# Kernel optimization log

Hardware: AMD Instinct MI355X
Metric: run time of the kernel (lower is better)

The kernel has to match this reference:

```python
import jax, jax.numpy as jnp
import numpy as np

N, A, C = 4, 8732, 81
SCALE_XY, SCALE_WH = 0.1, 0.2   # dboxes.scale_xy / scale_wh; Loss uses reciprocals
LAM, W_IOU = 1.0, 0.01
EPS_IOU = float(np.finfo(float).eps)


def setup_inputs() -> dict:
    key = jax.random.key(0)
    ks = jax.random.split(key, 8)
    ploc = jax.random.normal(ks[0], (N, 4, A), dtype=jnp.float32) * 0.5
    plabel = jax.random.normal(ks[1], (N, C, A), dtype=jnp.float32)
    # ground-truth loc in xywh with strictly positive wh (loc_vec takes a log)
    gxy = jax.random.uniform(ks[2], (N, 2, A), dtype=jnp.float32)
    gwh = jax.random.uniform(ks[3], (N, 2, A), dtype=jnp.float32) * 0.4 + 0.05
    gloc = jnp.concatenate([gxy, gwh], axis=1)
    lab = jax.random.randint(ks[4], (N, A), 1, C)
    keep = jax.random.uniform(ks[5], (N, A)) < 0.02
    glabel = jnp.where(keep, lab, 0).astype(jnp.int32)
    # default boxes in xywh, shape [1, 4, A]
    dxy = jax.random.uniform(ks[6], (1, 2, A), dtype=jnp.float32)
    dwh = jax.random.uniform(ks[7], (1, 2, A), dtype=jnp.float32) * 0.45 + 0.05
    dboxes = jnp.concatenate([dxy, dwh], axis=1)
    return {"ploc": ploc, "plabel": plabel, "gloc": gloc, "glabel": glabel, "dboxes": dboxes}


def _decode_ltrb(loc, dboxes):
    """scale_back_batch: encoded [N,4,A] + dboxes xywh [1,4,A] -> ltrb [N,A,4]."""
    b = jnp.transpose(loc, (0, 2, 1))      # [N, A, 4]
    d = jnp.transpose(dboxes, (0, 2, 1))   # [1, A, 4]
    xy = SCALE_XY * b[..., :2] * d[..., 2:] + d[..., :2]
    wh = jnp.exp(SCALE_WH * b[..., 2:]) * d[..., 2:]
    return jnp.concatenate([xy - 0.5 * wh, xy + 0.5 * wh], axis=-1)


def _iou_sum(p, g):
    """p, g: [A,4] ltrb -> per-anchor sum over all g boxes of IoU(p_i, g_k)."""
    area_p = (p[:, 2] - p[:, 0]) * (p[:, 3] - p[:, 1])
    area_g = (g[:, 2] - g[:, 0]) * (g[:, 3] - g[:, 1])
    iw = jnp.maximum(jnp.minimum(p[:, None, 2], g[None, :, 2]) - jnp.maximum(p[:, None, 0], g[None, :, 0]), 0.0)
    ih = jnp.maximum(jnp.minimum(p[:, None, 3], g[None, :, 3]) - jnp.maximum(p[:, None, 1], g[None, :, 1]), 0.0)
    inter = iw * ih                                      # [A, A]
    ua = jnp.maximum(area_p[:, None] + area_g[None, :] - inter, EPS_IOU)
    return (inter / ua).sum(axis=1)                      # [A]


def _forward(ploc, plabel, gloc, glabel, dboxes):
    mask = glabel > 0                                    # [N, A]
    pos_num = mask.sum(axis=1)                           # [N]

    # loc_vec: encode ground truth against default boxes
    dxy, dwh = dboxes[:, :2, :], dboxes[:, 2:, :]
    gxy_t = (1.0 / SCALE_XY) * (gloc[:, :2, :] - dxy) / dwh
    gwh_t = (1.0 / SCALE_WH) * jnp.log(gloc[:, 2:, :] / dwh)
    vec_gd = jnp.concatenate([gxy_t, gwh_t], axis=1)     # [N, 4, A]

    # SmoothL1 (beta=1), summed over coord dim
    diff = ploc - vec_gd
    ad = jnp.abs(diff)
    sl1 = jnp.where(ad < 1.0, 0.5 * diff * diff, ad - 0.5).sum(axis=1)  # [N, A]

    # per-anchor cross entropy
    logp = jax.nn.log_softmax(plabel, axis=1)            # [N, C, A]
    con = -jnp.take_along_axis(logp, glabel[:, None, :], axis=1)[:, 0, :]  # [N, A]

    # weighted-IoU reweighting (weights are detached in the original)
    p_ltrb = _decode_ltrb(ploc, dboxes)                  # [N, A, 4]
    g_ltrb = _decode_ltrb(gloc, dboxes)
    iou_s = jax.vmap(_iou_sum)(p_ltrb, g_ltrb)           # [N, A]
    valid = (p_ltrb[..., 0] < p_ltrb[..., 2]) & (p_ltrb[..., 1] < p_ltrb[..., 3])
    weights = jnp.where(valid, W_IOU * iou_s ** LAM, 0.0)
    weights = jax.lax.stop_gradient(weights)
    sl1 = (sl1 / (sl1 + weights)) * sl1

    sl1_pos = (mask.astype(sl1.dtype) * sl1).sum(axis=1)  # [N]

    # hard negative mining: double argsort for ranks
    con_neg = jnp.where(mask, 0.0, con)
    con_idx = jnp.argsort(-con_neg, axis=1)
    con_rank = jnp.argsort(con_idx, axis=1)
    neg_num = jnp.minimum(3 * pos_num, A)[:, None]
    neg_mask = con_rank < neg_num
    closs = (con * (mask.astype(con.dtype) + neg_mask.astype(con.dtype))).sum(axis=1)

    total = sl1_pos + closs
    num_mask = (pos_num > 0).astype(total.dtype)
    pn = jnp.maximum(pos_num.astype(total.dtype), 1e-6)
    return (total * num_mask / pn).mean()


def reference(ploc, plabel, gloc, glabel, dboxes):
    return _forward(ploc, plabel, gloc, glabel, dboxes)
```

## Files before the change

### kernel.cpp

```cpp
#include <hip/hip_runtime.h>
#include <math.h>

#define A_N 8732
#define NAT (4 * A_N)
#define BATCH 4
#define CLS 81
#define TILE 256
#define PTHREADS 512
#define SEG 128
#define ABLKP 69
#define NBINS 2048
#define PLB 128

__device__ __forceinline__ float sl1f(float d) {
    float ad = fabsf(d);
    return ad < 1.0f ? 0.5f * d * d : ad - 0.5f;
}
__device__ __forceinline__ unsigned umap(float v) {
    return __float_as_uint(v) | 0x80000000u;
}

__device__ void suffix_find(const int* lcnt, const float* lsum, int k, int tid,
                            int* ic, float* fsum,
                            int* o_b, int* o_krem, float* o_sumA)
{
    int base = tid * 8;
    int cs = 0; float ss = 0.0f;
    #pragma unroll
    for (int j = 0; j < 8; j++) { cs += lcnt[base + j]; ss += lsum[base + j]; }
    ic[tid] = cs; fsum[tid] = ss;
    __syncthreads();
    for (int off = 1; off < TILE; off <<= 1) {
        int v = ic[tid]; float f = fsum[tid];
        int v2 = 0; float f2 = 0.0f;
        if (tid + off < TILE) { v2 = ic[tid + off]; f2 = fsum[tid + off]; }
        __syncthreads();
        ic[tid] = v + v2; fsum[tid] = f + f2;
        __syncthreads();
    }
    int run = ic[tid] - cs;
    float runs = fsum[tid] - ss;
    for (int j = 7; j >= 0; j--) {
        int b = base + j; int c = lcnt[b];
        if (run < k && run + c >= k) { *o_b = b; *o_krem = k - run; *o_sumA = runs; }
        run += c; runs += lsum[b];
    }
    __syncthreads();
}

__global__ __launch_bounds__(PTHREADS) void prep_kernel(
    const float* __restrict__ ploc, const float* __restrict__ plabel,
    const float* __restrict__ gloc, const int* __restrict__ glabel,
    const float* __restrict__ dboxes,
    float4* __restrict__ pbox, float4* __restrict__ gbox,
    float* __restrict__ sl1raw, float* __restrict__ conneg,
    int* __restrict__ poslist,
    int* __restrict__ poscnt,
    float* __restrict__ consum,
    float* __restrict__ out)
{
    __shared__ float sh_se[4][SEG];
    __shared__ float sh_xg[4][SEG];
    __shared__ int   wcnt[2];
    __shared__ float wsum[2];
    const int t   = threadIdx.x;
    const int blk = blockIdx.x;
    const int n   = blockIdx.y;
    const int i     = t & (SEG - 1);
    const int chunk = t >> 7;
    const int a = blk * SEG + i;

    if (t == 0 && blk == 0 && n == 0) *out = 0.0f;

    int lab = 0;
    float se = 0.0f, xv = 0.0f;
    if (a < A_N) {
        lab = glabel[n * A_N + a];
        const float* pb = plabel + (size_t)n * CLS * A_N + a;
        const int c0 = chunk * 20 + (chunk > 0 ? 1 : 0);
        const int c1 = c0 + (chunk == 0 ? 21 : 20);
        #pragma unroll 21
        for (int c = c0; c < c1; c++) {
            float x = pb[(size_t)c * A_N];
            se += expf(x);
            xv = (c == lab) ? x : xv;
        }
    }
    sh_se[chunk][i] = se;
    sh_xg[chunk][i] = xv;
    __syncthreads();

    bool msk = false;
    float cv = 0.0f;
    if (t < SEG && a < A_N) {
        float set = sh_se[0][i] + sh_se[1][i] + sh_se[2][i] + sh_se[3][i];
        float xg  = sh_xg[0][i] + sh_xg[1][i] + sh_xg[2][i] + sh_xg[3][i];
        cv = logf(set) - xg;
        msk = lab > 0;
        conneg[n * A_N + a] = msk ? 0.0f : cv;

        float d0 = dboxes[0*A_N+a], d1 = dboxes[1*A_N+a], d2 = dboxes[2*A_N+a], d3 = dboxes[3*A_N+a];
        const float* pl = ploc + (size_t)n * 4 * A_N;
        const float* gl = gloc + (size_t)n * 4 * A_N;
        float p0 = pl[0*A_N+a], p1 = pl[1*A_N+a], p2 = pl[2*A_N+a], p3 = pl[3*A_N+a];
        float g0 = gl[0*A_N+a], g1 = gl[1*A_N+a], g2 = gl[2*A_N+a], g3 = gl[3*A_N+a];

        float v0 = 10.0f * (g0 - d0) / d2;
        float v1 = 10.0f * (g1 - d1) / d3;
        float v2 = 5.0f * logf(g2 / d2);
        float v3 = 5.0f * logf(g3 / d3);
        sl1raw[n * A_N + a] = sl1f(p0-v0) + sl1f(p1-v1) + sl1f(p2-v2) + sl1f(p3-v3);

        float cx = 0.1f*p0*d2 + d0, cy = 0.1f*p1*d3 + d1;
        float cw = expf(0.2f*p2)*d2, ch = expf(0.2f*p3)*d3;
        pbox[(size_t)n*A_N + a] = make_float4(cx-0.5f*cw, cy-0.5f*ch, cx+0.5f*cw, cy+0.5f*ch);
        float ex = 0.1f*g0*d2 + d0, ey = 0.1f*g1*d3 + d1;
        float ew = expf(0.2f*g2)*d2, eh = expf(0.2f*g3)*d3;
        gbox[(size_t)n*A_N + a] = make_float4(ex-0.5f*ew, ey-0.5f*eh, ex+0.5f*ew, ey+0.5f*eh);
    }

    unsigned long long bal = __ballot(msk);
    int wid = t >> 6, lane = t & 63;
    float wv = msk ? cv : 0.0f;
    #pragma unroll
    for (int off = 32; off > 0; off >>= 1) wv += __shfl_down(wv, off);
    if (t < SEG && lane == 0) { wcnt[wid] = __popcll(bal); wsum[wid] = wv; }
    __syncthreads();
    if (msk) {
        int base = (wid == 1) ? wcnt[0] : 0;
        int off = base + (int)__popcll(bal & ((1ULL << lane) - 1ULL));
        poslist[(n * ABLKP + blk) * SEG + off] = a;
    }
    if (t == 0) {
        poscnt[n * ABLKP + blk] = wcnt[0] + wcnt[1];
        consum[n * ABLKP + blk] = wsum[0] + wsum[1];
    }
}

__global__ __launch_bounds__(TILE) void tail_kernel(
    const float4* __restrict__ pbox, const float4* __restrict__ gbox,
    const float* __restrict__ sl1raw, const float* __restrict__ conneg,
    const int* __restrict__ poslist, const int* __restrict__ poscnt,
    const float* __restrict__ consum,
    float* __restrict__ out)
{
    __shared__ int   spre[ABLKP + 1];
    __shared__ float r4[4];
    const int n = blockIdx.y, tid = threadIdx.x;

    if (tid == 0) {
        int run = 0;
        #pragma unroll
        for (int s = 0; s < ABLKP; s++) { spre[s] = run; run += poscnt[n * ABLKP + s]; }
        spre[ABLKP] = run;
    }
    __syncthreads();
    const int np = spre[ABLKP];
    if (np <= 0) return;
    const float inv = 1.0f / ((float)np * (float)BATCH);

    if (blockIdx.x < PLB) {
        for (int p = blockIdx.x; p < np; p += PLB) {
            int s = 0;
            while (spre[s + 1] <= p) s++;
            int a = poslist[(n * ABLKP + s) * SEG + (p - spre[s])];
            float4 b = pbox[(size_t)n * A_N + a];
            float ap = (b.z - b.x) * (b.w - b.y);
            float acc = 0.0f;
            for (int k = tid; k < A_N; k += TILE) {
                float4 g = gbox[(size_t)n * A_N + k];
                float iw = fmaxf(fminf(b.z, g.z) - fmaxf(b.x, g.x), 0.0f);
                float ih = fmaxf(fminf(b.w, g.w) - fmaxf(b.y, g.y), 0.0f);
                float inter = iw * ih;
                float ua = ap + (g.z - g.x) * (g.w - g.y) - inter;
                acc += inter * __builtin_amdgcn_rcpf(ua);
            }
            #pragma unroll
            for (int off = 32; off > 0; off >>= 1) acc += __shfl_down(acc, off);
            if ((tid & 63) == 0) r4[tid >> 6] = acc;
            __syncthreads();
            if (tid == 0) {
                float iou = r4[0] + r4[1] + r4[2] + r4[3];
                bool valid = (b.x < b.z) && (b.y < b.w);
                float w = valid ? 0.01f * iou : 0.0f;
                float sv = sl1raw[n * A_N + a];
                atomicAdd(out, (sv / (sv + w) * sv) * inv);
            }
            __syncthreads();
        }
    } else {
        __shared__ int   lcnt[NBINS];
        __shared__ float lsum[NBINS];
        __shared__ int   ic[TILE];
        __shared__ float fs_[TILE];
        __shared__ int sb1, skrem1, sb2, skrem2;
        __shared__ float ssA1, ssA2;
        int k = min(3 * np, A_N);

        const float4* cn4 = (const float4*)(conneg + (size_t)n * A_N);

        for (int b = tid; b < NBINS; b += TILE) { lcnt[b] = 0; lsum[b] = 0.0f; }
        __syncthreads();
        for (int i = tid; i < A_N / 4; i += TILE) {
            float4 v = cn4[i];
            #pragma unroll
            for (int j = 0; j < 4; j++) {
                float vv = (j == 0) ? v.x : (j == 1) ? v.y : (j == 2) ? v.z : v.w;
                int d = (umap(vv) >> 20) & (NBINS - 1);
                atomicAdd(&lcnt[d], 1);
                atomicAdd(&lsum[d], vv);
            }
        }
        __syncthreads();
        suffix_find(lcnt, lsum, k, tid, ic, fs_, &sb1, &skrem1, &ssA1);
        int b1 = sb1;
        __syncthreads();

        for (int b = tid; b < NBINS; b += TILE) { lcnt[b] = 0; lsum[b] = 0.0f; }
        __syncthreads();
        for (int i = tid; i < A_N / 4; i += TILE) {
            float4 v = cn4[i];
            #pragma unroll
            for (int j = 0; j < 4; j++) {
                float vv = (j == 0) ? v.x : (j == 1) ? v.y : (j == 2) ? v.z : v.w;
                unsigned u = umap(vv);
                if ((int)((u >> 20) & (NBINS - 1)) == b1) {
                    int d = (u >> 9) & (NBINS - 1);
                    atomicAdd(&lcnt[d], 1);
                    atomicAdd(&lsum[d], vv);
                }
            }
        }
        __syncthreads();
        suffix_find(lcnt, lsum, skrem1, tid, ic, fs_, &sb2, &skrem2, &ssA2);

        if (tid == 0) {
            float conpos = 0.0f;
            #pragma unroll
            for (int s = 0; s < ABLKP; s++) conpos += consum[n * ABLKP + s];
            unsigned ubin = 0x80000000u | ((unsigned)sb1 << 20) | ((unsigned)sb2 << 9) | 256u;
            float tval = __uint_as_float(ubin & 0x7fffffffu);
            float closs_neg = ssA1 + ssA2 + (float)skrem2 * tval;
            atomicAdd(out, (conpos + closs_neg) * inv);
        }
    }
}

extern "C" void kernel_launch(void* const* d_in, const int* in_sizes, int n_in,
                              void* d_out, int out_size, void* d_ws, size_t ws_size,
                              hipStream_t stream) {
    const float* ploc   = (const float*)d_in[0];
    const float* plabel = (const float*)d_in[1];
    const float* gloc   = (const float*)d_in[2];
    const int*   glabel = (const int*)d_in[3];
    const float* dboxes = (const float*)d_in[4];
    float* out = (float*)d_out;

    float4* pbox    = (float4*)d_ws;
    float4* gbox    = pbox + NAT;
    float*  sl1raw  = (float*)(gbox + NAT);
    float*  conneg  = sl1raw + NAT;
    int*    poslist = (int*)(conneg + NAT);
    int*    poscnt  = poslist + BATCH * ABLKP * SEG;
    float*  consum  = (float*)(poscnt + BATCH * ABLKP);

    prep_kernel<<<dim3(ABLKP, BATCH), PTHREADS, 0, stream>>>(
        ploc, plabel, gloc, glabel, dboxes,
        pbox, gbox, sl1raw, conneg, poslist, poscnt, consum, out);
    tail_kernel<<<dim3(PLB + 1, BATCH), TILE, 0, stream>>>(
        pbox, gbox, sl1raw, conneg, poslist, poscnt, consum, out);
}
```

Measured before the change: 105.4 us.

## Shrink prep blocks to one wave; use shuffle scans and LDS caching in tail

The prep kernel now uses 64-anchor segments, so the per-segment ballot, compaction and reduction stay inside a single wave and need no shared-memory combine. In the tail kernel, suffix_find replaces the shared-memory Hillis-Steele scan, which had many barriers, with wave shuffles plus a 4-entry cross-wave fixup. The selection block caches conneg in LDS so the second histogram pass does not reread global memory. Loading poscnt and reducing consum are now done in parallel instead of by a single thread. The trade-off is that the number of segment blocks doubles and the selection block uses about 35KB more LDS.

After: 107.8 us. +2.3%, slower.

```diff
diff --git a/kernel.cpp b/kernel.cpp
--- a/kernel.cpp
+++ b/kernel.cpp
@@ -6,9 +6,9 @@
 #define BATCH 4
 #define CLS 81
 #define TILE 256
-#define PTHREADS 512
-#define SEG 128
-#define ABLKP 69
+#define PTHREADS 256
+#define SEG 64
+#define ABLKP 137
 #define NBINS 2048
 #define PLB 128
 
@@ -20,30 +20,31 @@
     return __float_as_uint(v) | 0x80000000u;
 }
 
-__device__ void suffix_find(const int* lcnt, const float* lsum, int k, int tid,
-                            int* ic, float* fsum,
-                            int* o_b, int* o_krem, float* o_sumA)
+__device__ __forceinline__ void suffix_find(const int* lcnt, const float* lsum,
+        int k, int tid, int* wtc, float* wts,
+        int* o_b, int* o_krem, float* o_sumA)
 {
-    int base = tid * 8;
+    const int base = tid * 8;
     int cs = 0; float ss = 0.0f;
     #pragma unroll
     for (int j = 0; j < 8; j++) { cs += lcnt[base + j]; ss += lsum[base + j]; }
-    ic[tid] = cs; fsum[tid] = ss;
-    __syncthreads();
-    for (int off = 1; off < TILE; off <<= 1) {
-        int v = ic[tid]; float f = fsum[tid];
-        int v2 = 0; float f2 = 0.0f;
-        if (tid + off < TILE) { v2 = ic[tid + off]; f2 = fsum[tid + off]; }
-        __syncthreads();
-        ic[tid] = v + v2; fsum[tid] = f + f2;
-        __syncthreads();
-    }
-    int run = ic[tid] - cs;
-    float runs = fsum[tid] - ss;
+    int c = cs; float s = ss;
+    const int lane = tid & 63;
+    #pragma unroll
+    for (int off = 1; off < 64; off <<= 1) {
+        int c2 = __shfl_down(c, off); float s2 = __shfl_down(s, off);
+        if (lane + off < 64) { c += c2; s += s2; }
+    }
+    const int wid = tid >> 6;
+    if (lane == 0) { wtc[wid] = c; wts[wid] = s; }
+    __syncthreads();
+    int run = c - cs; float runs = s - ss;
+    #pragma unroll
+    for (int w = 0; w < 4; w++) if (w > wid) { run += wtc[w]; runs += wts[w]; }
     for (int j = 7; j >= 0; j--) {
-        int b = base + j; int c = lcnt[b];
-        if (run < k && run + c >= k) { *o_b = b; *o_krem = k - run; *o_sumA = runs; }
-        run += c; runs += lsum[b];
+        int b = base + j; int cb = lcnt[b];
+        if (run < k && run + cb >= k) { *o_b = b; *o_krem = k - run; *o_sumA = runs; }
+        run += cb; runs += lsum[b];
     }
     __syncthreads();
 }
@@ -61,14 +62,12 @@
 {
     __shared__ float sh_se[4][SEG];
     __shared__ float sh_xg[4][SEG];
-    __shared__ int   wcnt[2];
-    __shared__ float wsum[2];
-    const int t   = threadIdx.x;
-    const int blk = blockIdx.x;
-    const int n   = blockIdx.y;
-    const int i     = t & (SEG - 1);
-    const int chunk = t >> 7;
-    const int a = blk * SEG + i;
+    const int t     = threadIdx.x;
+    const int blk   = blockIdx.x;
+    const int n     = blockIdx.y;
+    const int i     = t & 63;
+    const int chunk = t >> 6;
+    const int a     = blk * SEG + i;
 
     if (t == 0 && blk == 0 && n == 0) *out = 0.0f;
 
@@ -90,50 +89,47 @@
     sh_xg[chunk][i] = xv;
     __syncthreads();
 
-    bool msk = false;
-    float cv = 0.0f;
-    if (t < SEG && a < A_N) {
-        float set = sh_se[0][i] + sh_se[1][i] + sh_se[2][i] + sh_se[3][i];
-        float xg  = sh_xg[0][i] + sh_xg[1][i] + sh_xg[2][i] + sh_xg[3][i];
-        cv = logf(set) - xg;
-        msk = lab > 0;
-        conneg[n * A_N + a] = msk ? 0.0f : cv;
-
-        float d0 = dboxes[0*A_N+a], d1 = dboxes[1*A_N+a], d2 = dboxes[2*A_N+a], d3 = dboxes[3*A_N+a];
-        const float* pl = ploc + (size_t)n * 4 * A_N;
-        const float* gl = gloc + (size_t)n * 4 * A_N;
-        float p0 = pl[0*A_N+a], p1 = pl[1*A_N+a], p2 = pl[2*A_N+a], p3 = pl[3*A_N+a];
-        float g0 = gl[0*A_N+a], g1 = gl[1*A_N+a], g2 = gl[2*A_N+a], g3 = gl[3*A_N+a];
-
-        float v0 = 10.0f * (g0 - d0) / d2;
-        float v1 = 10.0f * (g1 - d1) / d3;
-        float v2 = 5.0f * logf(g2 / d2);
-        float v3 = 5.0f * logf(g3 / d3);
-        sl1raw[n * A_N + a] = sl1f(p0-v0) + sl1f(p1-v1) + sl1f(p2-v2) + sl1f(p3-v3);
-
-        float cx = 0.1f*p0*d2 + d0, cy = 0.1f*p1*d3 + d1;
-        float cw = expf(0.2f*p2)*d2, ch = expf(0.2f*p3)*d3;
-        pbox[(size_t)n*A_N + a] = make_float4(cx-0.5f*cw, cy-0.5f*ch, cx+0.5f*cw, cy+0.5f*ch);
-        float ex = 0.1f*g0*d2 + d0, ey = 0.1f*g1*d3 + d1;
-        float ew = expf(0.2f*g2)*d2, eh = expf(0.2f*g3)*d3;
-        gbox[(size_t)n*A_N + a] = make_float4(ex-0.5f*ew, ey-0.5f*eh, ex+0.5f*ew, ey+0.5f*eh);
-    }
-
-    unsigned long long bal = __ballot(msk);
-    int wid = t >> 6, lane = t & 63;
-    float wv = msk ? cv : 0.0f;
-    #pragma unroll
-    for (int off = 32; off > 0; off >>= 1) wv += __shfl_down(wv, off);
-    if (t < SEG && lane == 0) { wcnt[wid] = __popcll(bal); wsum[wid] = wv; }
-    __syncthreads();
-    if (msk) {
-        int base = (wid == 1) ? wcnt[0] : 0;
-        int off = base + (int)__popcll(bal & ((1ULL << lane) - 1ULL));
-        poslist[(n * ABLKP + blk) * SEG + off] = a;
-    }
-    if (t == 0) {
-        poscnt[n * ABLKP + blk] = wcnt[0] + wcnt[1];
-        consum[n * ABLKP + blk] = wsum[0] + wsum[1];
+    if (t < SEG) {
+        bool msk = false;
+        float cv = 0.0f;
+        if (a < A_N) {
+            float set = sh_se[0][i] + sh_se[1][i] + sh_se[2][i] + sh_se[3][i];
+            float xg  = sh_xg[0][i] + sh_xg[1][i] + sh_xg[2][i] + sh_xg[3][i];
+            cv = logf(set) - xg;
+            msk = lab > 0;
+            conneg[n * A_N + a] = msk ? 0.0f : cv;
+
+            float d0 = dboxes[0*A_N+a], d1 = dboxes[1*A_N+a], d2 = dboxes[2*A_N+a], d3 = dboxes[3*A_N+a];
+            const float* pl = ploc + (size_t)n * 4 * A_N;
+            const float* gl = gloc + (size_t)n * 4 * A_N;
+            float p0 = pl[0*A_N+a], p1 = pl[1*A_N+a], p2 = pl[2*A_N+a], p3 = pl[3*A_N+a];
+            float g0 = gl[0*A_N+a], g1 = gl[1*A_N+a], g2 = gl[2*A_N+a], g3 = gl[3*A_N+a];
+
+            float v0 = 10.0f * (g0 - d0) / d2;
+            float v1 = 10.0f * (g1 - d1) / d3;
+            float v2 = 5.0f * logf(g2 / d2);
+            float v3 = 5.0f * logf(g3 / d3);
+            sl1raw[n * A_N + a] = sl1f(p0-v0) + sl1f(p1-v1) + sl1f(p2-v2) + sl1f(p3-v3);
+
+            float cx = 0.1f*p0*d2 + d0, cy = 0.1f*p1*d3 + d1;
+            float cw = expf(0.2f*p2)*d2, ch = expf(0.2f*p3)*d3;
+            pbox[(size_t)n*A_N + a] = make_float4(cx-0.5f*cw, cy-0.5f*ch, cx+0.5f*cw, cy+0.5f*ch);
+            float ex = 0.1f*g0*d2 + d0, ey = 0.1f*g1*d3 + d1;
+            float ew = expf(0.2f*g2)*d2, eh = expf(0.2f*g3)*d3;
+            gbox[(size_t)n*A_N + a] = make_float4(ex-0.5f*ew, ey-0.5f*eh, ex+0.5f*ew, ey+0.5f*eh);
+        }
+        unsigned long long bal = __ballot(msk);
+        float wv = msk ? cv : 0.0f;
+        #pragma unroll
+        for (int off = 32; off > 0; off >>= 1) wv += __shfl_down(wv, off);
+        if (msk) {
+            int off2 = (int)__popcll(bal & ((1ULL << i) - 1ULL));
+            poslist[(n * ABLKP + blk) * SEG + off2] = a;
+        }
+        if (t == 0) {
+            poscnt[n * ABLKP + blk] = (int)__popcll(bal);
+            consum[n * ABLKP + blk] = wv;
+        }
     }
 }
 
@@ -145,13 +141,16 @@
     float* __restrict__ out)
 {
     __shared__ int   spre[ABLKP + 1];
+    __shared__ int   pv_[ABLKP];
     __shared__ float r4[4];
     const int n = blockIdx.y, tid = threadIdx.x;
 
+    if (tid < ABLKP) pv_[tid] = poscnt[n * ABLKP + tid];
+    __syncthreads();
     if (tid == 0) {
         int run = 0;
-        #pragma unroll
-        for (int s = 0; s < ABLKP; s++) { spre[s] = run; run += poscnt[n * ABLKP + s]; }
+        #pragma unroll 8
+        for (int s = 0; s < ABLKP; s++) { spre[s] = run; run += pv_[s]; }
         spre[ABLKP] = run;
     }
     __syncthreads();
@@ -189,10 +188,11 @@
             __syncthreads();
         }
     } else {
+        __shared__ float cnv[A_N];
         __shared__ int   lcnt[NBINS];
         __shared__ float lsum[NBINS];
-        __shared__ int   ic[TILE];
-        __shared__ float fs_[TILE];
+        __shared__ int   wtc[4];
+        __shared__ float wts[4];
         __shared__ int sb1, skrem1, sb2, skrem2;
         __shared__ float ssA1, ssA2;
         int k = min(3 * np, A_N);
@@ -206,38 +206,39 @@
             #pragma unroll
             for (int j = 0; j < 4; j++) {
                 float vv = (j == 0) ? v.x : (j == 1) ? v.y : (j == 2) ? v.z : v.w;
+                cnv[i * 4 + j] = vv;
                 int d = (umap(vv) >> 20) & (NBINS - 1);
                 atomicAdd(&lcnt[d], 1);
                 atomicAdd(&lsum[d], vv);
             }
         }
         __syncthreads();
-        suffix_find(lcnt, lsum, k, tid, ic, fs_, &sb1, &skrem1, &ssA1);
+        suffix_find(lcnt, lsum, k, tid, wtc, wts, &sb1, &skrem1, &ssA1);
         int b1 = sb1;
         __syncthreads();
 
         for (int b = tid; b < NBINS; b += TILE) { lcnt[b] = 0; lsum[b] = 0.0f; }
         __syncthreads();
-        for (int i = tid; i < A_N / 4; i += TILE) {
-            float4 v = cn4[i];
-            #pragma unroll
-            for (int j = 0; j < 4; j++) {
-                float vv = (j == 0) ? v.x : (j == 1) ? v.y : (j == 2) ? v.z : v.w;
-                unsigned u = umap(vv);
-                if ((int)((u >> 20) & (NBINS - 1)) == b1) {
-                    int d = (u >> 9) & (NBINS - 1);
-                    atomicAdd(&lcnt[d], 1);
-                    atomicAdd(&lsum[d], vv);
-                }
-            }
-        }
-        __syncthreads();
-        suffix_find(lcnt, lsum, skrem1, tid, ic, fs_, &sb2, &skrem2, &ssA2);
-
+        for (int i = tid; i < A_N; i += TILE) {
+            float vv = cnv[i];
+            unsigned u = umap(vv);
+            if ((int)((u >> 20) & (NBINS - 1)) == b1) {
+                int d = (u >> 9) & (NBINS - 1);
+                atomicAdd(&lcnt[d], 1);
+                atomicAdd(&lsum[d], vv);
+            }
+        }
+        __syncthreads();
+        suffix_find(lcnt, lsum, skrem1, tid, wtc, wts, &sb2, &skrem2, &ssA2);
+
+        float cp = 0.0f;
+        if (tid < ABLKP) cp = consum[n * ABLKP + tid];
+        #pragma unroll
+        for (int off = 32; off > 0; off >>= 1) cp += __shfl_down(cp, off);
+        if ((tid & 63) == 0) r4[tid >> 6] = cp;
+        __syncthreads();
         if (tid == 0) {
-            float conpos = 0.0f;
-            #pragma unroll
-            for (int s = 0; s < ABLKP; s++) conpos += consum[n * ABLKP + s];
+            float conpos = r4[0] + r4[1] + r4[2] + r4[3];
             unsigned ubin = 0x80000000u | ((unsigned)sb1 << 20) | ((unsigned)sb2 << 9) | 256u;
             float tval = __uint_as_float(ubin & 0x7fffffffu);
             float closs_neg = ssA1 + ssA2 + (float)skrem2 * tval;
```
